# Optimization experiments

Hardware: AMD Instinct MI355X
Metric: run time of the kernel (lower is better)

The kernel has to match this reference:

```python
import jax, jax.numpy as jnp
from jax import lax
import numpy as np

B, T, D = 256, 1000, 256
S, H = 10, 64  # num_tv segments, hidden size


def setup_inputs() -> dict:
    key = jax.random.key(0)
    ks = jax.random.split(key, 7)
    scale = 1.0 / np.sqrt(H)  # matches nn.RNN default uniform(-1/sqrt(H), 1/sqrt(H)) magnitude
    return {
        "x": jax.random.normal(ks[0], (B, T, D), dtype=jnp.float32),
        "W_ih": jax.random.normal(ks[1], (S, H, D), dtype=jnp.float32) * scale,
        "W_hh": jax.random.normal(ks[2], (S, H, H), dtype=jnp.float32) * scale,
        "b_ih": jax.random.normal(ks[3], (S, H), dtype=jnp.float32) * scale,
        "b_hh": jax.random.normal(ks[4], (S, H), dtype=jnp.float32) * scale,
        "fc_w": jax.random.normal(ks[5], (S, H), dtype=jnp.float32) * scale,
        "fc_b": jax.random.normal(ks[6], (S,), dtype=jnp.float32) * scale,
    }


def reference(x, W_ih, W_hh, b_ih, b_hh, fc_w, fc_b):
    # x: [B, T, D]; T split into S equal chunks of C steps; hidden state chained across segments.
    Bb, Tt, Dd = x.shape
    Ss = W_ih.shape[0]
    C = Tt // Ss
    Hh = W_ih.shape[1]

    # Per-segment input projection, done once as a big GEMM: [S, B, C, H]
    xr = x.reshape(Bb, Ss, C, Dd).transpose(1, 0, 2, 3)  # [S, B, C, D]
    xp = jnp.einsum('sbcd,shd->sbch', xr, W_ih) + b_ih[:, None, None, :]

    def seg_step(h, seg):
        xp_s, Whh, bhh = seg  # xp_s: [B, C, H]

        def t_step(h_prev, xt):  # xt: [B, H]
            h_new = jnp.tanh(xt + h_prev @ Whh.T + bhh)
            return h_new, h_new

        h_last, ys = lax.scan(t_step, h, jnp.swapaxes(xp_s, 0, 1))  # ys: [C, B, H]
        return h_last, ys

    h0 = jnp.zeros((Bb, Hh), dtype=x.dtype)
    _, ys = lax.scan(seg_step, h0, (xp, W_hh, b_hh))  # ys: [S, C, B, H]

    # Per-segment linear head Linear(H, 1), concat over time, sigmoid.
    y = jnp.einsum('scbh,sh->scb', ys, fc_w) + fc_b[:, None, None]  # [S, C, B]
    y = y.reshape(Ss * C, Bb).T[..., None]  # [B, T, 1]
    return jax.nn.sigmoid(y)
```

## Files before the change

### kernel.cpp

```cpp
#include <hip/hip_runtime.h>
#include <cstdint>

#define BB 256
#define TT 1000
#define DD 256
#define SS 10
#define HH 64
#define CC 100

#define PRE 2.885390081777927f

typedef float f32x2 __attribute__((ext_vector_type(2)));
typedef float f32x4 __attribute__((ext_vector_type(4)));

__global__ __launch_bounds__(256) void proj_kernel(
    const float* __restrict__ x, const float* __restrict__ W_ih,
    const float* __restrict__ b_ih, const float* __restrict__ b_hh,
    float* __restrict__ xp) {
  __shared__ float As[64][68];
  __shared__ float Bs[64][68];
  const int s = blockIdx.y;
  const int r0 = blockIdx.x * 64;
  const int tid = threadIdx.x;
  const int ty = tid >> 4, tx = tid & 15;
  const int ty4 = ty * 4, tx4 = tx * 4;
  float acc[4][4] = {{0.f, 0.f, 0.f, 0.f}};

  for (int kc = 0; kc < 4; ++kc) {
#pragma unroll
    for (int m = 0; m < 4; ++m) {
      int f = m * 256 + tid;
      int row = f >> 4, kq = f & 15;
      int r = r0 + row;
      int b = r / CC, c = r - b * CC;
      const float4 av = *(const float4*)(
          x + ((size_t)b * TT + s * CC + c) * DD + kc * 64 + kq * 4);
      *(float4*)&As[row][kq * 4] = av;
      const float4 wv = *(const float4*)(
          W_ih + ((size_t)s * HH + row) * DD + kc * 64 + kq * 4);
      *(float4*)&Bs[row][kq * 4] = wv;
    }
    __syncthreads();
#pragma unroll 4
    for (int k = 0; k < 64; k += 4) {
      float4 a[4], w[4];
#pragma unroll
      for (int i = 0; i < 4; ++i) a[i] = *(const float4*)&As[ty4 + i][k];
#pragma unroll
      for (int j = 0; j < 4; ++j) w[j] = *(const float4*)&Bs[tx4 + j][k];
#pragma unroll
      for (int i = 0; i < 4; ++i)
#pragma unroll
        for (int j = 0; j < 4; ++j)
          acc[i][j] += a[i].x * w[j].x + a[i].y * w[j].y +
                       a[i].z * w[j].z + a[i].w * w[j].w;
    }
    __syncthreads();
  }

  const float4 b1 = *(const float4*)(b_ih + s * HH + tx4);
  const float4 b2 = *(const float4*)(b_hh + s * HH + tx4);
#pragma unroll
  for (int i = 0; i < 4; ++i) {
    int r = r0 + ty4 + i;
    int b = r / CC, c = r - b * CC;
    float4 o;
    o.x = PRE * (acc[i][0] + b1.x + b2.x);
    o.y = PRE * (acc[i][1] + b1.y + b2.y);
    o.z = PRE * (acc[i][2] + b1.z + b2.z);
    o.w = PRE * (acc[i][3] + b1.w + b2.w);
    *(float4*)(xp + ((size_t)b * TT + s * CC + c) * HH + tx4) = o;
  }
}

__global__ __launch_bounds__(64, 1) void rnn_kernel(
    const float* __restrict__ xp, const float* __restrict__ W_hh,
    const float* __restrict__ fc_w, const float* __restrict__ fc_b,
    float* __restrict__ y) {
  __shared__ float hist[CC][68];
  const int b = blockIdx.x;
  const int lane = threadIdx.x;
  hist[CC - 1][lane] = 0.f;

  f32x2 Wp[32];
  float h = 0.f;
  for (int s = 0; s < SS; ++s) {
    const float* wr = W_hh + ((size_t)s * HH + lane) * HH;
#pragma unroll
    for (int j = 0; j < 16; ++j) {
      float4 v = *(const float4*)(wr + 4 * j);
      Wp[2 * j]     = (f32x2){PRE * v.x, PRE * v.y};
      Wp[2 * j + 1] = (f32x2){PRE * v.z, PRE * v.w};
    }
    const float* xps = xp + ((size_t)b * TT + s * CC) * HH + lane;

    float xq0 = xps[0 * HH];
    float xq1 = xps[1 * HH];
    float xq2 = xps[2 * HH];
    float xq3 = xps[3 * HH];

    for (int c4 = 0; c4 < 25; ++c4) {
#pragma unroll
      for (int u = 0; u < 4; ++u) {
        const int c = c4 * 4 + u;
        const int cp = (c == 0) ? CC - 1 : c - 1;
        const float xv = (u == 0) ? xq0 : (u == 1) ? xq1 : (u == 2) ? xq2 : xq3;
        f32x2 acc0 = {xv, 0.f};
        f32x2 acc1 = {0.f, 0.f};
#pragma unroll
        for (int j4 = 0; j4 < 16; ++j4) {
          const f32x4 hv = *(const f32x4*)&hist[cp][j4 * 4];
          const f32x2 lo = __builtin_shufflevector(hv, hv, 0, 1);
          const f32x2 hi = __builtin_shufflevector(hv, hv, 2, 3);
          acc0 = __builtin_elementwise_fma(Wp[2 * j4], lo, acc0);
          acc1 = __builtin_elementwise_fma(Wp[2 * j4 + 1], hi, acc1);
        }
        const f32x2 t = acc0 + acc1;
        const float z2 = t.x + t.y;
        const float e = __builtin_amdgcn_exp2f(z2);
        h = 1.f - 2.f * __builtin_amdgcn_rcpf(e + 1.f);
        hist[c][lane] = h;
        if (c4 < 24) {
          const float xn = xps[(c + 4) * HH];
          if (u == 0) xq0 = xn;
          else if (u == 1) xq1 = xn;
          else if (u == 2) xq2 = xn;
          else xq3 = xn;
        }
      }
    }

    const float fb = fc_b[s];
    const float* fw = fc_w + s * HH;
#pragma unroll
    for (int base = 0; base < CC; base += 64) {
      int l = base + lane;
      if (l < CC) {
        float z = fb;
#pragma unroll
        for (int i = 0; i < 64; i += 4) {
          const float4 hv = *(const float4*)&hist[l][i];
          z += hv.x * fw[i] + hv.y * fw[i + 1] + hv.z * fw[i + 2] +
               hv.w * fw[i + 3];
        }
        y[(size_t)b * TT + s * CC + l] =
            __builtin_amdgcn_rcpf(1.f + __expf(-z));
      }
    }
  }
}

extern "C" void kernel_launch(void* const* d_in, const int* in_sizes, int n_in,
                              void* d_out, int out_size, void* d_ws,
                              size_t ws_size, hipStream_t stream) {
  const float* x    = (const float*)d_in[0];
  const float* W_ih = (const float*)d_in[1];
  const float* W_hh = (const float*)d_in[2];
  const float* b_ih = (const float*)d_in[3];
  const float* b_hh = (const float*)d_in[4];
  const float* fc_w = (const float*)d_in[5];
  const float* fc_b = (const float*)d_in[6];
  float* y  = (float*)d_out;
  float* xp = (float*)d_ws;

  proj_kernel<<<dim3(400, 10), 256, 0, stream>>>(x, W_ih, b_ih, b_hh, xp);
  rnn_kernel<<<256, 64, 0, stream>>>(xp, W_hh, fc_w, fc_b, y);
}
```

Baseline: 353.6 us.

## Fuse input projection into RNN kernel, overlapping next-segment projection with recurrence

Replaces the separate projection GEMM plus recurrence kernels with one 512-thread block per batch row. Wave 0 runs the serial recurrence for segment s. The other seven waves compute the input projection for segment s+1 into a double-buffered LDS tile, splitting K across waves and combining partial sums with LDS atomicAdd. This removes the global round trip through the xp workspace and one kernel launch, and hides the projection behind the latency-bound recurrence. The risk is that projection waves compete for issue slots and LDS bandwidth with the critical recurrence wave, and the LDS atomics add contention.

```diff
diff --git a/kernel.cpp b/kernel.cpp
--- a/kernel.cpp
+++ b/kernel.cpp
@@ -7,146 +7,168 @@
 #define SS 10
 #define HH 64
 #define CC 100
-
 #define PRE 2.885390081777927f
 
 typedef float f32x2 __attribute__((ext_vector_type(2)));
 typedef float f32x4 __attribute__((ext_vector_type(4)));
 
-__global__ __launch_bounds__(256) void proj_kernel(
+__device__ __forceinline__ f32x2 lo2(f32x4 v) {
+  return __builtin_shufflevector(v, v, 0, 1);
+}
+__device__ __forceinline__ f32x2 hi2(f32x4 v) {
+  return __builtin_shufflevector(v, v, 2, 3);
+}
+
+__device__ __forceinline__ void proj_seg(
     const float* __restrict__ x, const float* __restrict__ W_ih,
-    const float* __restrict__ b_ih, const float* __restrict__ b_hh,
-    float* __restrict__ xp) {
-  __shared__ float As[64][68];
-  __shared__ float Bs[64][68];
-  const int s = blockIdx.y;
-  const int r0 = blockIdx.x * 64;
-  const int tid = threadIdx.x;
-  const int ty = tid >> 4, tx = tid & 15;
-  const int ty4 = ty * 4, tx4 = tx * 4;
-  float acc[4][4] = {{0.f, 0.f, 0.f, 0.f}};
+    float (*__restrict__ dst)[66], int b, int sp, int w, int lane) {
+  const int ko = (w == 1) ? 0 : (40 + 36 * (w - 2));
+  const bool full = (w == 1);
 
-  for (int kc = 0; kc < 4; ++kc) {
+  f32x2 Wk[20];
+  const float* wrow = W_ih + ((size_t)sp * HH + lane) * DD + ko;
 #pragma unroll
-    for (int m = 0; m < 4; ++m) {
-      int f = m * 256 + tid;
-      int row = f >> 4, kq = f & 15;
-      int r = r0 + row;
-      int b = r / CC, c = r - b * CC;
-      const float4 av = *(const float4*)(
-          x + ((size_t)b * TT + s * CC + c) * DD + kc * 64 + kq * 4);
-      *(float4*)&As[row][kq * 4] = av;
-      const float4 wv = *(const float4*)(
-          W_ih + ((size_t)s * HH + row) * DD + kc * 64 + kq * 4);
-      *(float4*)&Bs[row][kq * 4] = wv;
-    }
-    __syncthreads();
-#pragma unroll 4
-    for (int k = 0; k < 64; k += 4) {
-      float4 a[4], w[4];
-#pragma unroll
-      for (int i = 0; i < 4; ++i) a[i] = *(const float4*)&As[ty4 + i][k];
-#pragma unroll
-      for (int j = 0; j < 4; ++j) w[j] = *(const float4*)&Bs[tx4 + j][k];
-#pragma unroll
-      for (int i = 0; i < 4; ++i)
-#pragma unroll
-        for (int j = 0; j < 4; ++j)
-          acc[i][j] += a[i].x * w[j].x + a[i].y * w[j].y +
-                       a[i].z * w[j].z + a[i].w * w[j].w;
-    }
-    __syncthreads();
+  for (int q = 0; q < 9; ++q) {
+    const f32x4 v = *(const f32x4*)(wrow + 4 * q);
+    Wk[2 * q]     = (f32x2){PRE * v.x, PRE * v.y};
+    Wk[2 * q + 1] = (f32x2){PRE * v.z, PRE * v.w};
+  }
+  if (full) {
+    const f32x4 v = *(const f32x4*)(wrow + 36);
+    Wk[18] = (f32x2){PRE * v.x, PRE * v.y};
+    Wk[19] = (f32x2){PRE * v.z, PRE * v.w};
   }
 
-  const float4 b1 = *(const float4*)(b_ih + s * HH + tx4);
-  const float4 b2 = *(const float4*)(b_hh + s * HH + tx4);
+  const float* xr = x + ((size_t)b * TT + (size_t)sp * CC) * DD + ko;
+  f32x4 xa[10], xb[10];
 #pragma unroll
-  for (int i = 0; i < 4; ++i) {
-    int r = r0 + ty4 + i;
-    int b = r / CC, c = r - b * CC;
-    float4 o;
-    o.x = PRE * (acc[i][0] + b1.x + b2.x);
-    o.y = PRE * (acc[i][1] + b1.y + b2.y);
-    o.z = PRE * (acc[i][2] + b1.z + b2.z);
-    o.w = PRE * (acc[i][3] + b1.w + b2.w);
-    *(float4*)(xp + ((size_t)b * TT + s * CC + c) * HH + tx4) = o;
+  for (int q = 0; q < 9; ++q) xa[q] = *(const f32x4*)(xr + 4 * q);
+  if (full) xa[9] = *(const f32x4*)(xr + 36);
+
+  for (int c2 = 0; c2 < CC; c2 += 2) {
+    const float* xr1 = xr + (size_t)(c2 + 1) * DD;
+#pragma unroll
+    for (int q = 0; q < 9; ++q) xb[q] = *(const f32x4*)(xr1 + 4 * q);
+    if (full) xb[9] = *(const f32x4*)(xr1 + 36);
+    {
+      f32x2 a0 = {0.f, 0.f}, a1 = {0.f, 0.f};
+#pragma unroll
+      for (int q = 0; q < 9; ++q) {
+        a0 = __builtin_elementwise_fma(Wk[2 * q], lo2(xa[q]), a0);
+        a1 = __builtin_elementwise_fma(Wk[2 * q + 1], hi2(xa[q]), a1);
+      }
+      if (full) {
+        a0 = __builtin_elementwise_fma(Wk[18], lo2(xa[9]), a0);
+        a1 = __builtin_elementwise_fma(Wk[19], hi2(xa[9]), a1);
+      }
+      const f32x2 t = a0 + a1;
+      atomicAdd(&dst[c2][lane], t.x + t.y);
+    }
+    if (c2 + 2 < CC) {
+      const float* xr2 = xr + (size_t)(c2 + 2) * DD;
+#pragma unroll
+      for (int q = 0; q < 9; ++q) xa[q] = *(const f32x4*)(xr2 + 4 * q);
+      if (full) xa[9] = *(const f32x4*)(xr2 + 36);
+    }
+    {
+      f32x2 a0 = {0.f, 0.f}, a1 = {0.f, 0.f};
+#pragma unroll
+      for (int q = 0; q < 9; ++q) {
+        a0 = __builtin_elementwise_fma(Wk[2 * q], lo2(xb[q]), a0);
+        a1 = __builtin_elementwise_fma(Wk[2 * q + 1], hi2(xb[q]), a1);
+      }
+      if (full) {
+        a0 = __builtin_elementwise_fma(Wk[18], lo2(xb[9]), a0);
+        a1 = __builtin_elementwise_fma(Wk[19], hi2(xb[9]), a1);
+      }
+      const f32x2 t = a0 + a1;
+      atomicAdd(&dst[c2 + 1][lane], t.x + t.y);
+    }
   }
 }
 
-__global__ __launch_bounds__(64, 1) void rnn_kernel(
-    const float* __restrict__ xp, const float* __restrict__ W_hh,
-    const float* __restrict__ fc_w, const float* __restrict__ fc_b,
-    float* __restrict__ y) {
-  __shared__ float hist[CC][68];
+__global__ __launch_bounds__(512, 1) void fused_kernel(
+    const float* __restrict__ x, const float* __restrict__ W_ih,
+    const float* __restrict__ W_hh, const float* __restrict__ b_ih,
+    const float* __restrict__ b_hh, const float* __restrict__ fc_w,
+    const float* __restrict__ fc_b, float* __restrict__ y) {
+  __shared__ float buf[2][CC][66];
+  __shared__ float hrow[64];
   const int b = blockIdx.x;
-  const int lane = threadIdx.x;
-  hist[CC - 1][lane] = 0.f;
+  const int tid = threadIdx.x;
+  const int lane = tid & 63;
+  const int w = tid >> 6;
 
-  f32x2 Wp[32];
-  float h = 0.f;
+  if (tid < 64) hrow[tid] = 0.f;
+  for (int i = tid; i < CC * HH; i += 512) {
+    const int c = i >> 6, hh = i & 63;
+    buf[0][c][hh] = PRE * (b_ih[hh] + b_hh[hh]);
+  }
+  __syncthreads();
+  if (w >= 1) proj_seg(x, W_ih, buf[0], b, 0, w, lane);
+  __syncthreads();
+
   for (int s = 0; s < SS; ++s) {
-    const float* wr = W_hh + ((size_t)s * HH + lane) * HH;
+    const int p = s & 1;
+    if (s + 1 < SS) {
+      for (int i = tid; i < CC * HH; i += 512) {
+        const int c = i >> 6, hh = i & 63;
+        buf[1 - p][c][hh] =
+            PRE * (b_ih[(s + 1) * HH + hh] + b_hh[(s + 1) * HH + hh]);
+      }
+    }
+    __syncthreads();
+
+    if (w == 0) {
+      f32x2 Wp[32];
+      const float* wr = W_hh + ((size_t)s * HH + lane) * HH;
 #pragma unroll
-    for (int j = 0; j < 16; ++j) {
-      float4 v = *(const float4*)(wr + 4 * j);
-      Wp[2 * j]     = (f32x2){PRE * v.x, PRE * v.y};
-      Wp[2 * j + 1] = (f32x2){PRE * v.z, PRE * v.w};
-    }
-    const float* xps = xp + ((size_t)b * TT + s * CC) * HH + lane;
-
-    float xq0 = xps[0 * HH];
-    float xq1 = xps[1 * HH];
-    float xq2 = xps[2 * HH];
-    float xq3 = xps[3 * HH];
-
-    for (int c4 = 0; c4 < 25; ++c4) {
-#pragma unroll
-      for (int u = 0; u < 4; ++u) {
-        const int c = c4 * 4 + u;
-        const int cp = (c == 0) ? CC - 1 : c - 1;
-        const float xv = (u == 0) ? xq0 : (u == 1) ? xq1 : (u == 2) ? xq2 : xq3;
-        f32x2 acc0 = {xv, 0.f};
-        f32x2 acc1 = {0.f, 0.f};
+      for (int j = 0; j < 16; ++j) {
+        const f32x4 v = *(const f32x4*)(wr + 4 * j);
+        Wp[2 * j]     = (f32x2){PRE * v.x, PRE * v.y};
+        Wp[2 * j + 1] = (f32x2){PRE * v.z, PRE * v.w};
+      }
+      float h = 0.f;
+      float xq = buf[p][0][lane];
+#pragma unroll 4
+      for (int c = 0; c < CC; ++c) {
+        const float xq_next = buf[p][(c + 1 < CC) ? c + 1 : c][lane];
+        const float* hb = (c == 0) ? hrow : &buf[p][c - 1][0];
+        f32x2 a0 = {xq, 0.f}, a1 = {0.f, 0.f};
 #pragma unroll
         for (int j4 = 0; j4 < 16; ++j4) {
-          const f32x4 hv = *(const f32x4*)&hist[cp][j4 * 4];
-          const f32x2 lo = __builtin_shufflevector(hv, hv, 0, 1);
-          const f32x2 hi = __builtin_shufflevector(hv, hv, 2, 3);
-          acc0 = __builtin_elementwise_fma(Wp[2 * j4], lo, acc0);
-          acc1 = __builtin_elementwise_fma(Wp[2 * j4 + 1], hi, acc1);
+          const f32x4 hv = *(const f32x4*)(hb + 4 * j4);
+          a0 = __builtin_elementwise_fma(Wp[2 * j4], lo2(hv), a0);
+          a1 = __builtin_elementwise_fma(Wp[2 * j4 + 1], hi2(hv), a1);
         }
-        const f32x2 t = acc0 + acc1;
-        const float z2 = t.x + t.y;
-        const float e = __builtin_amdgcn_exp2f(z2);
+        const f32x2 t = a0 + a1;
+        const float e = __builtin_amdgcn_exp2f(t.x + t.y);
         h = 1.f - 2.f * __builtin_amdgcn_rcpf(e + 1.f);
-        hist[c][lane] = h;
-        if (c4 < 24) {
-          const float xn = xps[(c + 4) * HH];
-          if (u == 0) xq0 = xn;
-          else if (u == 1) xq1 = xn;
-          else if (u == 2) xq2 = xn;
-          else xq3 = xn;
+        buf[p][c][lane] = h;
+        xq = xq_next;
+      }
+      hrow[lane] = h;
+      const float fb = fc_b[s];
+      const float* fw = fc_w + s * HH;
+#pragma unroll
+      for (int base = 0; base < CC; base += 64) {
+        const int l = base + lane;
+        if (l < CC) {
+          float z = fb;
+#pragma unroll
+          for (int i = 0; i < 64; i += 4) {
+            const f32x4 hv = *(const f32x4*)&buf[p][l][i];
+            z += hv.x * fw[i] + hv.y * fw[i + 1] + hv.z * fw[i + 2] +
+                 hv.w * fw[i + 3];
+          }
+          y[(size_t)b * TT + s * CC + l] =
+              __builtin_amdgcn_rcpf(1.f + __expf(-z));
         }
       }
+    } else if (s + 1 < SS) {
+      proj_seg(x, W_ih, buf[1 - p], b, s + 1, w, lane);
     }
-
-    const float fb = fc_b[s];
-    const float* fw = fc_w + s * HH;
-#pragma unroll
-    for (int base = 0; base < CC; base += 64) {
-      int l = base + lane;
-      if (l < CC) {
-        float z = fb;
-#pragma unroll
-        for (int i = 0; i < 64; i += 4) {
-          const float4 hv = *(const float4*)&hist[l][i];
-          z += hv.x * fw[i] + hv.y * fw[i + 1] + hv.z * fw[i + 2] +
-               hv.w * fw[i + 3];
-        }
-        y[(size_t)b * TT + s * CC + l] =
-            __builtin_amdgcn_rcpf(1.f + __expf(-z));
-      }
-    }
+    __syncthreads();
   }
 }
 
@@ -160,9 +182,8 @@
   const float* b_hh = (const float*)d_in[4];
   const float* fc_w = (const float*)d_in[5];
   const float* fc_b = (const float*)d_in[6];
-  float* y  = (float*)d_out;
-  float* xp = (float*)d_ws;
+  float* y = (float*)d_out;
 
-  proj_kernel<<<dim3(400, 10), 256, 0, stream>>>(x, W_ih, b_ih, b_hh, xp);
-  rnn_kernel<<<256, 64, 0, stream>>>(xp, W_hh, fc_w, fc_b, y);
+  fused_kernel<<<256, 512, 0, stream>>>(x, W_ih, W_hh, b_ih, b_hh,
+                                        fc_w, fc_b, y);
 }
```

Measured after the change: 890.8 us. +151.9%, slower.

## Fuse projection and recurrence into one kernel with per-segment readiness flags

Applied to the files above, without the earlier changes.

Merges the input-projection GEMM and the RNN recurrence into a single launch. The first 256 blocks run the recurrence, and the remaining blocks compute projection tiles. Each projection block bumps an atomic counter for its segment when done, and recurrence blocks spin on that counter before reading the segment. This lets the recurrence of early segments overlap with projection of later ones, hiding most of the projection time and one launch boundary. The cost is an extra flag-zeroing launch and idle threads in the 256-wide recurrence blocks (only 64 lanes work). Correctness relies on projection blocks actually being scheduled while recurrence blocks spin; if they are not, the kernel deadlocks.

```diff
diff --git a/kernel.cpp b/kernel.cpp
--- a/kernel.cpp
+++ b/kernel.cpp
@@ -7,21 +7,24 @@
 #define SS 10
 #define HH 64
 #define CC 100
-
 #define PRE 2.885390081777927f
+#define PBS 400
 
 typedef float f32x2 __attribute__((ext_vector_type(2)));
 typedef float f32x4 __attribute__((ext_vector_type(4)));
 
-__global__ __launch_bounds__(256) void proj_kernel(
+__device__ __forceinline__ f32x2 lo2(f32x4 v) {
+  return __builtin_shufflevector(v, v, 0, 1);
+}
+__device__ __forceinline__ f32x2 hi2(f32x4 v) {
+  return __builtin_shufflevector(v, v, 2, 3);
+}
+
+__device__ __forceinline__ void proj_body(
     const float* __restrict__ x, const float* __restrict__ W_ih,
     const float* __restrict__ b_ih, const float* __restrict__ b_hh,
-    float* __restrict__ xp) {
-  __shared__ float As[64][68];
-  __shared__ float Bs[64][68];
-  const int s = blockIdx.y;
-  const int r0 = blockIdx.x * 64;
-  const int tid = threadIdx.x;
+    float* __restrict__ xp, int s, int r0, int tid,
+    float (*As)[68], float (*Bs)[68]) {
   const int ty = tid >> 4, tx = tid & 15;
   const int ty4 = ty * 4, tx4 = tx * 4;
   float acc[4][4] = {{0.f, 0.f, 0.f, 0.f}};
@@ -73,17 +76,14 @@
   }
 }
 
-__global__ __launch_bounds__(64, 1) void rnn_kernel(
+__device__ __forceinline__ void rnn_body(
     const float* __restrict__ xp, const float* __restrict__ W_hh,
     const float* __restrict__ fc_w, const float* __restrict__ fc_b,
-    float* __restrict__ y) {
-  __shared__ float hist[CC][68];
-  const int b = blockIdx.x;
-  const int lane = threadIdx.x;
+    float* __restrict__ y, int* flags, int b, int lane,
+    float (*hist)[68]) {
   hist[CC - 1][lane] = 0.f;
 
   f32x2 Wp[32];
-  float h = 0.f;
   for (int s = 0; s < SS; ++s) {
     const float* wr = W_hh + ((size_t)s * HH + lane) * HH;
 #pragma unroll
@@ -92,6 +92,11 @@
       Wp[2 * j]     = (f32x2){PRE * v.x, PRE * v.y};
       Wp[2 * j + 1] = (f32x2){PRE * v.z, PRE * v.w};
     }
+    if (flags) {
+      while (__hip_atomic_load(&flags[s], __ATOMIC_ACQUIRE,
+                               __HIP_MEMORY_SCOPE_AGENT) < PBS)
+        __builtin_amdgcn_s_sleep(2);
+    }
     const float* xps = xp + ((size_t)b * TT + s * CC) * HH + lane;
 
     float xq0 = xps[0 * HH];
@@ -99,6 +104,7 @@
     float xq2 = xps[2 * HH];
     float xq3 = xps[3 * HH];
 
+    float h = 0.f;
     for (int c4 = 0; c4 < 25; ++c4) {
 #pragma unroll
       for (int u = 0; u < 4; ++u) {
@@ -110,10 +116,8 @@
 #pragma unroll
         for (int j4 = 0; j4 < 16; ++j4) {
           const f32x4 hv = *(const f32x4*)&hist[cp][j4 * 4];
-          const f32x2 lo = __builtin_shufflevector(hv, hv, 0, 1);
-          const f32x2 hi = __builtin_shufflevector(hv, hv, 2, 3);
-          acc0 = __builtin_elementwise_fma(Wp[2 * j4], lo, acc0);
-          acc1 = __builtin_elementwise_fma(Wp[2 * j4 + 1], hi, acc1);
+          acc0 = __builtin_elementwise_fma(Wp[2 * j4], lo2(hv), acc0);
+          acc1 = __builtin_elementwise_fma(Wp[2 * j4 + 1], hi2(hv), acc1);
         }
         const f32x2 t = acc0 + acc1;
         const float z2 = t.x + t.y;
@@ -150,6 +154,56 @@
   }
 }
 
+__global__ __launch_bounds__(256, 1) void mega_kernel(
+    const float* __restrict__ x, const float* __restrict__ W_ih,
+    const float* __restrict__ W_hh, const float* __restrict__ b_ih,
+    const float* __restrict__ b_hh, const float* __restrict__ fc_w,
+    const float* __restrict__ fc_b, float* __restrict__ xp,
+    int* __restrict__ flags, float* __restrict__ y) {
+  __shared__ union {
+    struct { float As[64][68]; float Bs[64][68]; } p;
+    float hist[CC][68];
+  } sm;
+  const int bid = blockIdx.x;
+  const int tid = threadIdx.x;
+
+  if (bid >= BB) {
+    const int pb = bid - BB;
+    const int s = pb / PBS;
+    const int r0 = (pb % PBS) * 64;
+    proj_body(x, W_ih, b_ih, b_hh, xp, s, r0, tid, sm.p.As, sm.p.Bs);
+    __threadfence();
+    __syncthreads();
+    if (tid == 0)
+      __hip_atomic_fetch_add(&flags[s], 1, __ATOMIC_RELEASE,
+                             __HIP_MEMORY_SCOPE_AGENT);
+  } else {
+    if (tid >= 64) return;
+    rnn_body(xp, W_hh, fc_w, fc_b, y, flags, bid, tid, sm.hist);
+  }
+}
+
+__global__ void zero_flags(int* f) {
+  if (threadIdx.x < 16) f[threadIdx.x] = 0;
+}
+
+__global__ __launch_bounds__(256) void proj_kernel(
+    const float* __restrict__ x, const float* __restrict__ W_ih,
+    const float* __restrict__ b_ih, const float* __restrict__ b_hh,
+    float* __restrict__ xp) {
+  __shared__ float As[64][68];
+  __shared__ float Bs[64][68];
+  proj_body(x, W_ih, b_ih, b_hh, xp, blockIdx.y, blockIdx.x * 64,
+            threadIdx.x, As, Bs);
+}
+__global__ __launch_bounds__(64, 1) void rnn_kernel(
+    const float* __restrict__ xp, const float* __restrict__ W_hh,
+    const float* __restrict__ fc_w, const float* __restrict__ fc_b,
+    float* __restrict__ y) {
+  __shared__ float hist[CC][68];
+  rnn_body(xp, W_hh, fc_w, fc_b, y, nullptr, blockIdx.x, threadIdx.x, hist);
+}
+
 extern "C" void kernel_launch(void* const* d_in, const int* in_sizes, int n_in,
                               void* d_out, int out_size, void* d_ws,
                               size_t ws_size, hipStream_t stream) {
@@ -162,7 +216,15 @@
   const float* fc_b = (const float*)d_in[6];
   float* y  = (float*)d_out;
   float* xp = (float*)d_ws;
-
-  proj_kernel<<<dim3(400, 10), 256, 0, stream>>>(x, W_ih, b_ih, b_hh, xp);
-  rnn_kernel<<<256, 64, 0, stream>>>(xp, W_hh, fc_w, fc_b, y);
-}
+  const size_t XPB = (size_t)BB * TT * HH * sizeof(float);
+
+  if (ws_size >= XPB + 64) {
+    int* flags = (int*)((char*)d_ws + XPB);
+    zero_flags<<<1, 64, 0, stream>>>(flags);
+    mega_kernel<<<BB + SS * PBS, 256, 0, stream>>>(
+        x, W_ih, W_hh, b_ih, b_hh, fc_w, fc_b, xp, flags, y);
+  } else {
+    proj_kernel<<<dim3(PBS, SS), 256, 0, stream>>>(x, W_ih, b_ih, b_hh, xp);
+    rnn_kernel<<<BB, 64, 0, stream>>>(xp, W_hh, fc_w, fc_b, y);
+  }
+}
```

After: 1.248 ms. 253% more time.
